# Performance work log

Hardware: AMD Instinct MI355X
Metric: run time of the kernel (lower is better)

Reference implementation:

```python
import jax, jax.numpy as jnp
import numpy as np

N, A, M = 2, 360, 512
NP, PS = 32, 64


def _rampfilter(size):
    n = np.concatenate((np.arange(1, size / 2 + 1, 2, dtype=int),
                        np.arange(size / 2 - 1, 0, -2, dtype=int)))
    f = np.zeros(size)
    f[0] = 0.25
    f[1::2] = -1 / (np.pi * n) ** 2
    return 2 * np.real(np.fft.fft(f))


def setup_inputs() -> dict:
    rng = np.random.default_rng(0)
    sino = rng.standard_normal((N, 1, A, M))
    # ramp filtering (done in __init__ of the torch module, filtered=True)
    final_width = max(64, int(2 ** np.ceil(np.log2(2 * M))))
    pad = final_width - M
    filt = _rampfilter(final_width)
    sino_p = np.pad(sino, ((0, 0), (0, 0), (0, 0), (0, pad)))
    sino_f = np.real(np.fft.ifft(np.fft.fft(sino_p, axis=-1) * filt, axis=-1))[..., :M]
    # patch centers sampled uniformly inside the reconstruction circle
    cx, cy = [], []
    while sum(len(a) for a in cx) < NP:
        x_ = rng.random(NP) * M
        y_ = rng.random(NP) * M
        m = (x_ - M / 2) ** 2 + (y_ - M / 2) ** 2 <= (M / 2) ** 2
        cx.append(x_[m]); cy.append(y_[m])
    centers_x = np.concatenate(cx)[:NP]
    centers_y = np.concatenate(cy)[:NP]
    theta = np.linspace(0.0, np.pi, A, endpoint=False)
    return {
        'sinogram': jnp.asarray(sino_f, jnp.float32),
        'theta': jnp.asarray(theta, jnp.float32),
        'centers_x': jnp.asarray(centers_x, jnp.float32),
        'centers_y': jnp.asarray(centers_y, jnp.float32),
    }


def reference(sinogram, theta, centers_x, centers_y):
    n, _, a, m = sinogram.shape
    sino = sinogram[:, 0]                                  # (N, A, M)
    half = (m - 1) / 2.0
    x = jnp.arange(PS, dtype=sinogram.dtype) - PS / 2.0
    # patch grids (torch meshgrid 'ij'): gX varies along rows, gy along cols
    gX = (x[:, None] + jnp.zeros((PS,), sinogram.dtype)[None, :])[None] + centers_x[:, None, None]
    gy = (jnp.zeros((PS,), sinogram.dtype)[:, None] + x[None, :])[None] + centers_y[:, None, None]
    gX = gX / half - 1.0                                   # (NP, PS, PS), normalized
    gy = gy / half - 1.0
    ct, st = jnp.cos(theta), jnp.sin(theta)                # (A,)
    # rotated detector coordinate per angle: (NP, A, PS, PS)
    xg = gX[:, None] * ct[None, :, None, None] - gy[:, None] * st[None, :, None, None]
    # grid_sample bilinear along M with align_corners=True, zero padding
    u = (xg + 1.0) * half
    i0 = jnp.floor(u)
    w = u - i0
    i0i = i0.astype(jnp.int32)
    i1i = i0i + 1
    w0 = jnp.where((i0i >= 0) & (i0i <= m - 1), 1.0 - w, 0.0)
    w1 = jnp.where((i1i >= 0) & (i1i <= m - 1), w, 0.0)
    i0c = jnp.clip(i0i, 0, m - 1)
    i1c = jnp.clip(i1i, 0, m - 1)
    a_idx = jnp.arange(a)[None, :, None, None]
    g0 = sino[:, a_idx, i0c]                               # (N, NP, A, PS, PS)
    g1 = sino[:, a_idx, i1c]
    recon = (g0 * w0[None] + g1 * w1[None]).sum(axis=2)    # sum over angles -> (N, NP, PS, PS)
    mask = ((gX ** 2 + gy ** 2) <= 1.0).astype(recon.dtype)
    recon = recon * mask[None]
    return recon * (np.pi / (2.0 * a))
```

## Files before the change

kernel.cpp:

```cpp
#include <hip/hip_runtime.h>
#include <math.h>

#define N_  2
#define A_  360
#define M_  512
#define NP_ 32
#define PS_ 64
#define HALF_A 180
#define W_  24

__global__ __launch_bounds__(512) void fbp_kernel(
    const float* __restrict__ sino,
    const float* __restrict__ theta,
    const float* __restrict__ cxs,
    const float* __restrict__ cys,
    float* __restrict__ out)
{
    __shared__ float win[A_ * W_];
    __shared__ alignas(16) float csA[A_];
    __shared__ alignas(16) float syA[A_];
    __shared__ alignas(16) float ofA[A_];
    __shared__ float red[256];

    const float half = 255.5f;
    const int tid = threadIdx.x;

    const int bid    = blockIdx.x;
    const int region = bid & 15;
    const int p      = (bid >> 4) & (NP_ - 1);
    const int n      = bid >> 9;
    const int ri     = (region >> 2) << 4;
    const int rj     = (region &  3) << 4;

    const float cx = cxs[p];
    const float cy = cys[p];

    const float gX0 = ((float)(ri      - PS_ / 2) + cx) / half - 1.0f;
    const float gX1 = ((float)(ri + 15 - PS_ / 2) + cx) / half - 1.0f;
    const float gy0 = ((float)(rj      - PS_ / 2) + cy) / half - 1.0f;
    const float gy1 = ((float)(rj + 15 - PS_ / 2) + cy) / half - 1.0f;

    if (tid < A_) {
        const float th  = theta[tid];
        const float csx = cosf(th) * half;
        const float csy = sinf(th) * half;
        const float t0  = fmaf(-gy0, csy, half);
        const float t1  = fmaf(-gy1, csy, half);
        const float u00 = fmaf(gX0, csx, t0);
        const float u10 = fmaf(gX1, csx, t0);
        const float u01 = fmaf(gX0, csx, t1);
        const float u11 = fmaf(gX1, csx, t1);
        const float lof = floorf(fminf(fminf(u00, u10), fminf(u01, u11)));
        csA[tid] = csx;
        syA[tid] = csy;
        ofA[tid] = half - lof;
    }
    __syncthreads();

    const float* __restrict__ srow = sino + n * (A_ * M_);
    for (int e = tid; e < A_ * W_; e += 512) {
        const int a  = e / W_;
        const int k  = e - a * W_;
        const int lo = (int)(half - ofA[a]);
        const int idx = min(max(lo + k, 0), M_ - 1);
        win[e] = srow[a * M_ + idx];
    }
    __syncthreads();

    const int team = tid >> 8;
    const int t    = tid & 255;
    const int i    = ri + (t >> 4);
    const int j    = rj + (t & 15);

    const float gX  = ((float)(i - PS_ / 2) + cx) / half - 1.0f;
    const float gy  = ((float)(j - PS_ / 2) + cy) / half - 1.0f;
    const float ngy = -gy;

    const int gbase = team * (HALF_A / 4);
    const float4* __restrict__ cs4 = (const float4*)csA;
    const float4* __restrict__ sy4 = (const float4*)syA;
    const float4* __restrict__ of4 = (const float4*)ofA;

    float accG = 0.0f;
    float accW = 0.0f;
    const float* wp0 = win + team * (HALF_A * W_);

    #pragma unroll 3
    for (int g = 0; g < HALF_A / 4; ++g) {
        const float4 c4 = cs4[gbase + g];
        const float4 s4 = sy4[gbase + g];
        const float4 o4 = of4[gbase + g];
        const float* wp = wp0 + g * (4 * W_);

        {
            float u = fmaf(gX, c4.x, fmaf(ngy, s4.x, o4.x));
            u = fminf(fmaxf(u, 0.0f), 22.999f);
            const int   k = (int)u;
            const float w = __builtin_amdgcn_fractf(u);
            const float g0 = wp[k + 0 * W_], g1 = wp[k + 0 * W_ + 1];
            accG += g0;  accW = fmaf(w, g1 - g0, accW);
        }
        {
            float u = fmaf(gX, c4.y, fmaf(ngy, s4.y, o4.y));
            u = fminf(fmaxf(u, 0.0f), 22.999f);
            const int   k = (int)u;
            const float w = __builtin_amdgcn_fractf(u);
            const float g0 = wp[k + 1 * W_], g1 = wp[k + 1 * W_ + 1];
            accG += g0;  accW = fmaf(w, g1 - g0, accW);
        }
        {
            float u = fmaf(gX, c4.z, fmaf(ngy, s4.z, o4.z));
            u = fminf(fmaxf(u, 0.0f), 22.999f);
            const int   k = (int)u;
            const float w = __builtin_amdgcn_fractf(u);
            const float g0 = wp[k + 2 * W_], g1 = wp[k + 2 * W_ + 1];
            accG += g0;  accW = fmaf(w, g1 - g0, accW);
        }
        {
            float u = fmaf(gX, c4.w, fmaf(ngy, s4.w, o4.w));
            u = fminf(fmaxf(u, 0.0f), 22.999f);
            const int   k = (int)u;
            const float w = __builtin_amdgcn_fractf(u);
            const float g0 = wp[k + 3 * W_], g1 = wp[k + 3 * W_ + 1];
            accG += g0;  accW = fmaf(w, g1 - g0, accW);
        }
    }

    const float part = accG + accW;
    if (team == 1) red[t] = part;
    __syncthreads();
    if (team == 0) {
        const float inside = (fmaf(gX, gX, gy * gy) <= 1.0f) ? 1.0f : 0.0f;
        const float scale  = (float)(M_PI / (2.0 * (double)A_));
        out[(((n * NP_) + p) * PS_ + i) * PS_ + j] =
            (part + red[t]) * inside * scale;
    }
}

extern "C" void kernel_launch(void* const* d_in, const int* in_sizes, int n_in,
                              void* d_out, int out_size, void* d_ws, size_t ws_size,
                              hipStream_t stream) {
    const float* sino  = (const float*)d_in[0];
    const float* theta = (const float*)d_in[1];
    const float* cxs   = (const float*)d_in[2];
    const float* cys   = (const float*)d_in[3];
    float* out = (float*)d_out;

    const int blocks = N_ * NP_ * (PS_ * PS_ / 256);
    fbp_kernel<<<dim3(blocks), dim3(512), 0, stream>>>(sino, theta, cxs, cys, out);
}
```

Measured before the change: 28.98 us.

## Split angles between direct global gathers and LDS window with paired float2 samples

Each team now reads 88 of its 180 angles straight from global memory (via the cache) using unaligned 2-float vector loads, and stages only the remaining 92 angles into a smaller shared-memory window. The window stores adjacent sample pairs as float2, so each bilinear tap needs one LDS read instead of two. This is meant to cut LDS staging time and LDS read pressure by spreading the gather work across both the global/cache path and LDS. In exchange it adds global-memory latency inside the main loop and duplicates each staged sample. Out-of-range samples are handled by clamping rather than zero padding, which the reference does differently.

```diff
diff --git a/kernel.cpp b/kernel.cpp
--- a/kernel.cpp
+++ b/kernel.cpp
@@ -6,8 +6,13 @@
 #define M_  512
 #define NP_ 32
 #define PS_ 64
-#define HALF_A 180
-#define W_  24
+#define TEAM_A  180
+#define TA_ANG  88
+#define LDS_ANG 92
+#define NW      (2 * LDS_ANG)
+#define W_      24
+
+typedef float f2u __attribute__((ext_vector_type(2), aligned(4)));
 
 __global__ __launch_bounds__(512) void fbp_kernel(
     const float* __restrict__ sino,
@@ -16,10 +21,10 @@
     const float* __restrict__ cys,
     float* __restrict__ out)
 {
-    __shared__ float win[A_ * W_];
+    __shared__ float2 win2[NW * W_];
     __shared__ alignas(16) float csA[A_];
     __shared__ alignas(16) float syA[A_];
-    __shared__ alignas(16) float ofA[A_];
+    __shared__ alignas(16) float ofA[NW];
     __shared__ float red[256];
 
     const float half = 255.5f;
@@ -44,26 +49,32 @@
         const float th  = theta[tid];
         const float csx = cosf(th) * half;
         const float csy = sinf(th) * half;
-        const float t0  = fmaf(-gy0, csy, half);
-        const float t1  = fmaf(-gy1, csy, half);
-        const float u00 = fmaf(gX0, csx, t0);
-        const float u10 = fmaf(gX1, csx, t0);
-        const float u01 = fmaf(gX0, csx, t1);
-        const float u11 = fmaf(gX1, csx, t1);
-        const float lof = floorf(fminf(fminf(u00, u10), fminf(u01, u11)));
         csA[tid] = csx;
         syA[tid] = csy;
-        ofA[tid] = half - lof;
+        const int tm = (tid >= TEAM_A) ? 1 : 0;
+        const int al = tid - tm * TEAM_A;
+        if (al >= TA_ANG) {
+            const float t0  = fmaf(-gy0, csy, half);
+            const float t1  = fmaf(-gy1, csy, half);
+            const float u00 = fmaf(gX0, csx, t0);
+            const float u10 = fmaf(gX1, csx, t0);
+            const float u01 = fmaf(gX0, csx, t1);
+            const float u11 = fmaf(gX1, csx, t1);
+            const float lof = floorf(fminf(fminf(u00, u10), fminf(u01, u11)));
+            ofA[tm * LDS_ANG + (al - TA_ANG)] = half - lof;
+        }
     }
     __syncthreads();
 
     const float* __restrict__ srow = sino + n * (A_ * M_);
-    for (int e = tid; e < A_ * W_; e += 512) {
-        const int a  = e / W_;
-        const int k  = e - a * W_;
-        const int lo = (int)(half - ofA[a]);
-        const int idx = min(max(lo + k, 0), M_ - 1);
-        win[e] = srow[a * M_ + idx];
+    for (int e = tid; e < NW * W_; e += 512) {
+        const int w  = e / W_;
+        const int k  = e - w * W_;
+        const int a  = (w < LDS_ANG) ? (w + TA_ANG) : (w + TA_ANG + TA_ANG);
+        const int lo = (int)(half - ofA[w]);
+        const int i0 = min(max(lo + k,     0), M_ - 1);
+        const int i1 = min(max(lo + k + 1, 0), M_ - 1);
+        win2[e] = make_float2(srow[a * M_ + i0], srow[a * M_ + i1]);
     }
     __syncthreads();
 
@@ -76,53 +87,105 @@
     const float gy  = ((float)(j - PS_ / 2) + cy) / half - 1.0f;
     const float ngy = -gy;
 
-    const int gbase = team * (HALF_A / 4);
     const float4* __restrict__ cs4 = (const float4*)csA;
     const float4* __restrict__ sy4 = (const float4*)syA;
     const float4* __restrict__ of4 = (const float4*)ofA;
 
+    const int cs_base  = team * 45;
+    const int csl_base = team * 45 + 22;
+    const int of_base  = team * 23;
+    const float*  __restrict__ srowTA = srow + team * TEAM_A * M_;
+    const float2* __restrict__ wbase  = win2 + team * LDS_ANG * W_;
+
     float accG = 0.0f;
     float accW = 0.0f;
-    const float* wp0 = win + team * (HALF_A * W_);
-
-    #pragma unroll 3
-    for (int g = 0; g < HALF_A / 4; ++g) {
-        const float4 c4 = cs4[gbase + g];
-        const float4 s4 = sy4[gbase + g];
-        const float4 o4 = of4[gbase + g];
-        const float* wp = wp0 + g * (4 * W_);
-
-        {
-            float u = fmaf(gX, c4.x, fmaf(ngy, s4.x, o4.x));
-            u = fminf(fmaxf(u, 0.0f), 22.999f);
-            const int   k = (int)u;
-            const float w = __builtin_amdgcn_fractf(u);
-            const float g0 = wp[k + 0 * W_], g1 = wp[k + 0 * W_ + 1];
-            accG += g0;  accW = fmaf(w, g1 - g0, accW);
-        }
-        {
-            float u = fmaf(gX, c4.y, fmaf(ngy, s4.y, o4.y));
-            u = fminf(fmaxf(u, 0.0f), 22.999f);
-            const int   k = (int)u;
-            const float w = __builtin_amdgcn_fractf(u);
-            const float g0 = wp[k + 1 * W_], g1 = wp[k + 1 * W_ + 1];
-            accG += g0;  accW = fmaf(w, g1 - g0, accW);
-        }
-        {
-            float u = fmaf(gX, c4.z, fmaf(ngy, s4.z, o4.z));
-            u = fminf(fmaxf(u, 0.0f), 22.999f);
-            const int   k = (int)u;
-            const float w = __builtin_amdgcn_fractf(u);
-            const float g0 = wp[k + 2 * W_], g1 = wp[k + 2 * W_ + 1];
-            accG += g0;  accW = fmaf(w, g1 - g0, accW);
-        }
-        {
-            float u = fmaf(gX, c4.w, fmaf(ngy, s4.w, o4.w));
-            u = fminf(fmaxf(u, 0.0f), 22.999f);
-            const int   k = (int)u;
-            const float w = __builtin_amdgcn_fractf(u);
-            const float g0 = wp[k + 3 * W_], g1 = wp[k + 3 * W_ + 1];
-            accG += g0;  accW = fmaf(w, g1 - g0, accW);
+
+    #pragma unroll 2
+    for (int q = 0; q < 22; ++q) {
+        const float4 c4 = cs4[cs_base + q];
+        const float4 s4 = sy4[cs_base + q];
+        const float* r  = srowTA + (q * 4) * M_;
+
+        float u0 = fmaf(gX, c4.x, fmaf(ngy, s4.x, half));
+        float u1 = fmaf(gX, c4.y, fmaf(ngy, s4.y, half));
+        float u2 = fmaf(gX, c4.z, fmaf(ngy, s4.z, half));
+        float u3 = fmaf(gX, c4.w, fmaf(ngy, s4.w, half));
+        u0 = fminf(fmaxf(u0, 0.0f), 510.999f);
+        u1 = fminf(fmaxf(u1, 0.0f), 510.999f);
+        u2 = fminf(fmaxf(u2, 0.0f), 510.999f);
+        u3 = fminf(fmaxf(u3, 0.0f), 510.999f);
+        const f2u ga0 = *(const f2u*)(r + 0 * M_ + (int)u0);
+        const f2u ga1 = *(const f2u*)(r + 1 * M_ + (int)u1);
+        const f2u ga2 = *(const f2u*)(r + 2 * M_ + (int)u2);
+        const f2u ga3 = *(const f2u*)(r + 3 * M_ + (int)u3);
+        const float wa0 = __builtin_amdgcn_fractf(u0);
+        const float wa1 = __builtin_amdgcn_fractf(u1);
+        const float wa2 = __builtin_amdgcn_fractf(u2);
+        const float wa3 = __builtin_amdgcn_fractf(u3);
+
+        const float4 cl = cs4[csl_base + q];
+        const float4 sl = sy4[csl_base + q];
+        const float4 o4 = of4[of_base + q];
+        const float2* wp = wbase + (q * 4) * W_;
+        {
+            float u = fmaf(gX, cl.x, fmaf(ngy, sl.x, o4.x));
+            u = fminf(fmaxf(u, 0.0f), 22.999f);
+            const float2 g = wp[(int)u];
+            accG += g.x;  accW = fmaf(__builtin_amdgcn_fractf(u), g.y - g.x, accW);
+        }
+        {
+            float u = fmaf(gX, cl.y, fmaf(ngy, sl.y, o4.y));
+            u = fminf(fmaxf(u, 0.0f), 22.999f);
+            const float2 g = wp[W_ + (int)u];
+            accG += g.x;  accW = fmaf(__builtin_amdgcn_fractf(u), g.y - g.x, accW);
+        }
+        {
+            float u = fmaf(gX, cl.z, fmaf(ngy, sl.z, o4.z));
+            u = fminf(fmaxf(u, 0.0f), 22.999f);
+            const float2 g = wp[2 * W_ + (int)u];
+            accG += g.x;  accW = fmaf(__builtin_amdgcn_fractf(u), g.y - g.x, accW);
+        }
+        {
+            float u = fmaf(gX, cl.w, fmaf(ngy, sl.w, o4.w));
+            u = fminf(fmaxf(u, 0.0f), 22.999f);
+            const float2 g = wp[3 * W_ + (int)u];
+            accG += g.x;  accW = fmaf(__builtin_amdgcn_fractf(u), g.y - g.x, accW);
+        }
+
+        accG += ga0.x;  accW = fmaf(wa0, ga0.y - ga0.x, accW);
+        accG += ga1.x;  accW = fmaf(wa1, ga1.y - ga1.x, accW);
+        accG += ga2.x;  accW = fmaf(wa2, ga2.y - ga2.x, accW);
+        accG += ga3.x;  accW = fmaf(wa3, ga3.y - ga3.x, accW);
+    }
+
+    {
+        const float4 cl = cs4[csl_base + 22];
+        const float4 sl = sy4[csl_base + 22];
+        const float4 o4 = of4[of_base + 22];
+        const float2* wp = wbase + (22 * 4) * W_;
+        {
+            float u = fmaf(gX, cl.x, fmaf(ngy, sl.x, o4.x));
+            u = fminf(fmaxf(u, 0.0f), 22.999f);
+            const float2 g = wp[(int)u];
+            accG += g.x;  accW = fmaf(__builtin_amdgcn_fractf(u), g.y - g.x, accW);
+        }
+        {
+            float u = fmaf(gX, cl.y, fmaf(ngy, sl.y, o4.y));
+            u = fminf(fmaxf(u, 0.0f), 22.999f);
+            const float2 g = wp[W_ + (int)u];
+            accG += g.x;  accW = fmaf(__builtin_amdgcn_fractf(u), g.y - g.x, accW);
+        }
+        {
+            float u = fmaf(gX, cl.z, fmaf(ngy, sl.z, o4.z));
+            u = fminf(fmaxf(u, 0.0f), 22.999f);
+            const float2 g = wp[2 * W_ + (int)u];
+            accG += g.x;  accW = fmaf(__builtin_amdgcn_fractf(u), g.y - g.x, accW);
+        }
+        {
+            float u = fmaf(gX, cl.w, fmaf(ngy, sl.w, o4.w));
+            u = fminf(fmaxf(u, 0.0f), 22.999f);
+            const float2 g = wp[3 * W_ + (int)u];
+            accG += g.x;  accW = fmaf(__builtin_amdgcn_fractf(u), g.y - g.x, accW);
         }
     }
 
```

Result: slower. 32.54 us (+12.3%).

## Split angle groups between LDS windows and global pair-table gathers

Applied to the files above, without the earlier changes.

Adds a pre-pass kernel that builds (value, next-minus-value) pairs for the whole sinogram in workspace. The main kernel stages only half the angle groups into LDS, storing them as float2 pairs so each sample needs one LDS read. The other half is gathered straight from the global pair table through cache. This is meant to cut LDS staging and fill time and to overlap global gathers with LDS work, at the cost of an extra kernel launch, extra workspace traffic and scattered global loads. If the workspace is too small it falls back to the original LDS-only kernel.

```diff
diff --git a/kernel.cpp b/kernel.cpp
--- a/kernel.cpp
+++ b/kernel.cpp
@@ -6,14 +6,214 @@
 #define M_  512
 #define NP_ 32
 #define PS_ 64
-#define HALF_A 180
+#define TEAM_A 180
 #define W_  24
-
-__global__ __launch_bounds__(512) void fbp_kernel(
+#define LDSG 23
+#define NWANG (2 * LDSG * 4)
+
+__global__ __launch_bounds__(256) void make_pairs(
+    const float* __restrict__ sino, float2* __restrict__ pairs)
+{
+    const int idx = blockIdx.x * 256 + threadIdx.x;
+    const int k   = idx & (M_ - 1);
+    const float s0 = sino[idx];
+    const float s1 = (k < M_ - 1) ? sino[idx + 1] : s0;
+    pairs[idx] = make_float2(s0, s1 - s0);
+}
+
+__global__ __launch_bounds__(512) void fbp_split(
     const float* __restrict__ sino,
+    const float2* __restrict__ pairs,
     const float* __restrict__ theta,
     const float* __restrict__ cxs,
     const float* __restrict__ cys,
+    float* __restrict__ out)
+{
+    __shared__ float2 win2[NWANG * W_];
+    __shared__ alignas(16) float csA[A_];
+    __shared__ alignas(16) float syA[A_];
+    __shared__ alignas(16) float ofA[192];
+    __shared__ float red[256];
+
+    const float half = 255.5f;
+    const int tid = threadIdx.x;
+
+    const int bid    = blockIdx.x;
+    const int region = bid & 15;
+    const int p      = (bid >> 4) & (NP_ - 1);
+    const int n      = bid >> 9;
+    const int ri     = (region >> 2) << 4;
+    const int rj     = (region &  3) << 4;
+
+    const float cx = cxs[p];
+    const float cy = cys[p];
+
+    const float gX0 = ((float)(ri      - PS_ / 2) + cx) / half - 1.0f;
+    const float gX1 = ((float)(ri + 15 - PS_ / 2) + cx) / half - 1.0f;
+    const float gy0 = ((float)(rj      - PS_ / 2) + cy) / half - 1.0f;
+    const float gy1 = ((float)(rj + 15 - PS_ / 2) + cy) / half - 1.0f;
+
+    if (tid < A_) {
+        const float th  = theta[tid];
+        const float csx = cosf(th) * half;
+        const float csy = sinf(th) * half;
+        csA[tid] = csx;
+        syA[tid] = csy;
+        const int team = tid / TEAM_A;
+        const int al   = tid - team * TEAM_A;
+        const int g    = al >> 2;
+        if (!(g & 1)) {
+            const float t0  = fmaf(-gy0, csy, half);
+            const float t1  = fmaf(-gy1, csy, half);
+            const float u00 = fmaf(gX0, csx, t0);
+            const float u10 = fmaf(gX1, csx, t0);
+            const float u01 = fmaf(gX0, csx, t1);
+            const float u11 = fmaf(gX1, csx, t1);
+            const float lof = floorf(fminf(fminf(u00, u10), fminf(u01, u11)));
+            const int   wa  = (team * LDSG + (g >> 1)) * 4 + (al & 3);
+            ofA[wa] = half - lof;
+        }
+    }
+    __syncthreads();
+
+    const float* __restrict__ srow = sino + n * (A_ * M_);
+    for (int e = tid; e < NWANG * W_; e += 512) {
+        const int wa = e / W_;
+        const int k  = e - wa * W_;
+        const int tw = wa / (LDSG * 4);
+        const int r  = wa - tw * (LDSG * 4);
+        const int a  = tw * TEAM_A + ((r >> 2) << 3) + (r & 3);
+        const int lo = (int)(half - ofA[wa]);
+        const int i0 = min(max(lo + k,     0), M_ - 1);
+        const int i1 = min(max(lo + k + 1, 0), M_ - 1);
+        const float g0 = srow[a * M_ + i0];
+        const float g1 = srow[a * M_ + i1];
+        win2[e] = make_float2(g0, g1 - g0);
+    }
+    __syncthreads();
+
+    const int team = tid >> 8;
+    const int t    = tid & 255;
+    const int i    = ri + (t >> 4);
+    const int j    = rj + (t & 15);
+
+    const float gX  = ((float)(i - PS_ / 2) + cx) / half - 1.0f;
+    const float gy  = ((float)(j - PS_ / 2) + cy) / half - 1.0f;
+    const float ngy = -gy;
+
+    const float4* __restrict__ cs4 = (const float4*)csA;
+    const float4* __restrict__ sy4 = (const float4*)syA;
+    const float4* __restrict__ of4 = (const float4*)ofA;
+
+    const int     base_g  = team * 45;
+    const float2* wbase   = win2 + team * (LDSG * 4 * W_);
+    const float2* __restrict__ pairs_n = pairs + n * (A_ * M_);
+
+    float accG = 0.0f;
+    float accW = 0.0f;
+
+    #pragma unroll 2
+    for (int gg = 0; gg < 22; ++gg) {
+        const float4 cg = cs4[base_g + 2 * gg + 1];
+        const float4 sg = sy4[base_g + 2 * gg + 1];
+        float u0 = fmaf(gX, cg.x, fmaf(ngy, sg.x, half));
+        float u1 = fmaf(gX, cg.y, fmaf(ngy, sg.y, half));
+        float u2 = fmaf(gX, cg.z, fmaf(ngy, sg.z, half));
+        float u3 = fmaf(gX, cg.w, fmaf(ngy, sg.w, half));
+        u0 = fminf(fmaxf(u0, 0.0f), 510.999f);
+        u1 = fminf(fmaxf(u1, 0.0f), 510.999f);
+        u2 = fminf(fmaxf(u2, 0.0f), 510.999f);
+        u3 = fminf(fmaxf(u3, 0.0f), 510.999f);
+        const float2* pg = pairs_n + (team * TEAM_A + 8 * gg + 4) * M_;
+        const float2 pa = pg[(int)u0];
+        const float2 pb = pg[M_     + (int)u1];
+        const float2 pc = pg[2 * M_ + (int)u2];
+        const float2 pd = pg[3 * M_ + (int)u3];
+        const float w0 = __builtin_amdgcn_fractf(u0);
+        const float w1 = __builtin_amdgcn_fractf(u1);
+        const float w2 = __builtin_amdgcn_fractf(u2);
+        const float w3 = __builtin_amdgcn_fractf(u3);
+
+        const float4 cl = cs4[base_g + 2 * gg];
+        const float4 sl = sy4[base_g + 2 * gg];
+        const float4 o4 = of4[team * LDSG + gg];
+        const float2* wp = wbase + gg * (4 * W_);
+        {
+            float u = fmaf(gX, cl.x, fmaf(ngy, sl.x, o4.x));
+            u = fminf(fmaxf(u, 0.0f), 22.999f);
+            const float2 gg2 = wp[(int)u];
+            accG += gg2.x;  accW = fmaf(__builtin_amdgcn_fractf(u), gg2.y, accW);
+        }
+        {
+            float u = fmaf(gX, cl.y, fmaf(ngy, sl.y, o4.y));
+            u = fminf(fmaxf(u, 0.0f), 22.999f);
+            const float2 gg2 = wp[W_ + (int)u];
+            accG += gg2.x;  accW = fmaf(__builtin_amdgcn_fractf(u), gg2.y, accW);
+        }
+        {
+            float u = fmaf(gX, cl.z, fmaf(ngy, sl.z, o4.z));
+            u = fminf(fmaxf(u, 0.0f), 22.999f);
+            const float2 gg2 = wp[2 * W_ + (int)u];
+            accG += gg2.x;  accW = fmaf(__builtin_amdgcn_fractf(u), gg2.y, accW);
+        }
+        {
+            float u = fmaf(gX, cl.w, fmaf(ngy, sl.w, o4.w));
+            u = fminf(fmaxf(u, 0.0f), 22.999f);
+            const float2 gg2 = wp[3 * W_ + (int)u];
+            accG += gg2.x;  accW = fmaf(__builtin_amdgcn_fractf(u), gg2.y, accW);
+        }
+
+        accG += pa.x;  accW = fmaf(w0, pa.y, accW);
+        accG += pb.x;  accW = fmaf(w1, pb.y, accW);
+        accG += pc.x;  accW = fmaf(w2, pc.y, accW);
+        accG += pd.x;  accW = fmaf(w3, pd.y, accW);
+    }
+
+    {
+        const float4 cl = cs4[base_g + 44];
+        const float4 sl = sy4[base_g + 44];
+        const float4 o4 = of4[team * LDSG + 22];
+        const float2* wp = wbase + 22 * (4 * W_);
+        {
+            float u = fmaf(gX, cl.x, fmaf(ngy, sl.x, o4.x));
+            u = fminf(fmaxf(u, 0.0f), 22.999f);
+            const float2 gg2 = wp[(int)u];
+            accG += gg2.x;  accW = fmaf(__builtin_amdgcn_fractf(u), gg2.y, accW);
+        }
+        {
+            float u = fmaf(gX, cl.y, fmaf(ngy, sl.y, o4.y));
+            u = fminf(fmaxf(u, 0.0f), 22.999f);
+            const float2 gg2 = wp[W_ + (int)u];
+            accG += gg2.x;  accW = fmaf(__builtin_amdgcn_fractf(u), gg2.y, accW);
+        }
+        {
+            float u = fmaf(gX, cl.z, fmaf(ngy, sl.z, o4.z));
+            u = fminf(fmaxf(u, 0.0f), 22.999f);
+            const float2 gg2 = wp[2 * W_ + (int)u];
+            accG += gg2.x;  accW = fmaf(__builtin_amdgcn_fractf(u), gg2.y, accW);
+        }
+        {
+            float u = fmaf(gX, cl.w, fmaf(ngy, sl.w, o4.w));
+            u = fminf(fmaxf(u, 0.0f), 22.999f);
+            const float2 gg2 = wp[3 * W_ + (int)u];
+            accG += gg2.x;  accW = fmaf(__builtin_amdgcn_fractf(u), gg2.y, accW);
+        }
+    }
+
+    const float part = accG + accW;
+    if (team == 1) red[t] = part;
+    __syncthreads();
+    if (team == 0) {
+        const float inside = (fmaf(gX, gX, gy * gy) <= 1.0f) ? 1.0f : 0.0f;
+        const float scale  = (float)(M_PI / (2.0 * (double)A_));
+        out[(((n * NP_) + p) * PS_ + i) * PS_ + j] =
+            (part + red[t]) * inside * scale;
+    }
+}
+
+__global__ __launch_bounds__(512) void fbp_lds_only(
+    const float* __restrict__ sino, const float* __restrict__ theta,
+    const float* __restrict__ cxs,  const float* __restrict__ cys,
     float* __restrict__ out)
 {
     __shared__ float win[A_ * W_];
@@ -24,17 +224,14 @@
 
     const float half = 255.5f;
     const int tid = threadIdx.x;
-
     const int bid    = blockIdx.x;
     const int region = bid & 15;
     const int p      = (bid >> 4) & (NP_ - 1);
     const int n      = bid >> 9;
     const int ri     = (region >> 2) << 4;
     const int rj     = (region &  3) << 4;
-
     const float cx = cxs[p];
     const float cy = cys[p];
-
     const float gX0 = ((float)(ri      - PS_ / 2) + cx) / half - 1.0f;
     const float gX1 = ((float)(ri + 15 - PS_ / 2) + cx) / half - 1.0f;
     const float gy0 = ((float)(rj      - PS_ / 2) + cy) / half - 1.0f;
@@ -51,9 +248,7 @@
         const float u01 = fmaf(gX0, csx, t1);
         const float u11 = fmaf(gX1, csx, t1);
         const float lof = floorf(fminf(fminf(u00, u10), fminf(u01, u11)));
-        csA[tid] = csx;
-        syA[tid] = csy;
-        ofA[tid] = half - lof;
+        csA[tid] = csx;  syA[tid] = csy;  ofA[tid] = half - lof;
     }
     __syncthreads();
 
@@ -71,57 +266,53 @@
     const int t    = tid & 255;
     const int i    = ri + (t >> 4);
     const int j    = rj + (t & 15);
-
     const float gX  = ((float)(i - PS_ / 2) + cx) / half - 1.0f;
     const float gy  = ((float)(j - PS_ / 2) + cy) / half - 1.0f;
     const float ngy = -gy;
 
-    const int gbase = team * (HALF_A / 4);
+    const int gbase = team * (TEAM_A / 4);
     const float4* __restrict__ cs4 = (const float4*)csA;
     const float4* __restrict__ sy4 = (const float4*)syA;
     const float4* __restrict__ of4 = (const float4*)ofA;
-
-    float accG = 0.0f;
-    float accW = 0.0f;
-    const float* wp0 = win + team * (HALF_A * W_);
+    float accG = 0.0f, accW = 0.0f;
+    const float* wp0 = win + team * (TEAM_A * W_);
 
     #pragma unroll 3
-    for (int g = 0; g < HALF_A / 4; ++g) {
+    for (int g = 0; g < TEAM_A / 4; ++g) {
         const float4 c4 = cs4[gbase + g];
         const float4 s4 = sy4[gbase + g];
         const float4 o4 = of4[gbase + g];
         const float* wp = wp0 + g * (4 * W_);
-
         {
             float u = fmaf(gX, c4.x, fmaf(ngy, s4.x, o4.x));
             u = fminf(fmaxf(u, 0.0f), 22.999f);
-            const int   k = (int)u;
+            const int k = (int)u;
             const float w = __builtin_amdgcn_fractf(u);
-            const float g0 = wp[k + 0 * W_], g1 = wp[k + 0 * W_ + 1];
+            const float g0 = wp[k], g1 = wp[k + 1];
             accG += g0;  accW = fmaf(w, g1 - g0, accW);
         }
         {
             float u = fmaf(gX, c4.y, fmaf(ngy, s4.y, o4.y));
             u = fminf(fmaxf(u, 0.0f), 22.999f);
-            const int   k = (int)u;
+            const int k = (int)u;
             const float w = __builtin_amdgcn_fractf(u);
-            const float g0 = wp[k + 1 * W_], g1 = wp[k + 1 * W_ + 1];
+            const float g0 = wp[W_ + k], g1 = wp[W_ + k + 1];
             accG += g0;  accW = fmaf(w, g1 - g0, accW);
         }
         {
             float u = fmaf(gX, c4.z, fmaf(ngy, s4.z, o4.z));
             u = fminf(fmaxf(u, 0.0f), 22.999f);
-            const int   k = (int)u;
+            const int k = (int)u;
             const float w = __builtin_amdgcn_fractf(u);
-            const float g0 = wp[k + 2 * W_], g1 = wp[k + 2 * W_ + 1];
+            const float g0 = wp[2 * W_ + k], g1 = wp[2 * W_ + k + 1];
             accG += g0;  accW = fmaf(w, g1 - g0, accW);
         }
         {
             float u = fmaf(gX, c4.w, fmaf(ngy, s4.w, o4.w));
             u = fminf(fmaxf(u, 0.0f), 22.999f);
-            const int   k = (int)u;
+            const int k = (int)u;
             const float w = __builtin_amdgcn_fractf(u);
-            const float g0 = wp[k + 3 * W_], g1 = wp[k + 3 * W_ + 1];
+            const float g0 = wp[3 * W_ + k], g1 = wp[3 * W_ + k + 1];
             accG += g0;  accW = fmaf(w, g1 - g0, accW);
         }
     }
@@ -146,6 +337,14 @@
     const float* cys   = (const float*)d_in[3];
     float* out = (float*)d_out;
 
+    const size_t pairs_bytes = (size_t)N_ * A_ * M_ * sizeof(float2);
     const int blocks = N_ * NP_ * (PS_ * PS_ / 256);
-    fbp_kernel<<<dim3(blocks), dim3(512), 0, stream>>>(sino, theta, cxs, cys, out);
+
+    if (ws_size >= pairs_bytes) {
+        float2* pairs = (float2*)d_ws;
+        make_pairs<<<dim3(N_ * A_ * M_ / 256), dim3(256), 0, stream>>>(sino, pairs);
+        fbp_split<<<dim3(blocks), dim3(512), 0, stream>>>(sino, pairs, theta, cxs, cys, out);
+    } else {
+        fbp_lds_only<<<dim3(blocks), dim3(512), 0, stream>>>(sino, theta, cxs, cys, out);
+    }
 }
```

Measured after the change: 37.72 us. +30.1%, slower.
